# Optimization experiments

Hardware: AMD Instinct MI355X
Metric: run time of the kernel (lower is better)

The kernel has to match this reference:

```python
import jax, jax.numpy as jnp
import numpy as np

EPS = 1e-08

def setup_inputs() -> dict:
    key = jax.random.key(0)
    k1, k2 = jax.random.split(key)
    h = jax.random.normal(k1, (4096, 512), dtype=jnp.float32)   # [B, D]
    A = jax.random.normal(k2, (32768, 512), dtype=jnp.float32)  # [K, D]
    return {"h": h, "A": A}

def _l2_normalize(x, eps=EPS):
    # matches torch F.normalize(p=2): x / max(||x||, eps)
    n = jnp.sqrt(jnp.sum(x * x, axis=-1, keepdims=True))
    return x / jnp.maximum(n, eps)

def reference(h, A):
    # cosine metric: normalize both, matmul, argmax over K
    h_n = _l2_normalize(h)                      # [B, D]
    A_n = _l2_normalize(A)                      # [K, D]
    scores = jnp.einsum('bd,kd->bk', h_n, A_n)  # [B, K]
    idx = jnp.argmax(scores, axis=1, keepdims=True)  # [B, 1] int
    return idx
```

## Files before the change

kernel.cpp:

```cpp
#include <hip/hip_runtime.h>
#include <stdint.h>


#define DIM 512
#define B_ROWS 4096
#define K_ROWS 32768
#define BT 128
#define KT 128
#define NKT (K_ROWS / KT)
#define KSLOTS 32
#define NCHUNK 4
#define QSCALE (127.0f / 0.26f)

typedef __attribute__((ext_vector_type(4))) float fx4;
typedef __attribute__((ext_vector_type(4))) int int4v;
typedef unsigned long long u64;

__device__ __forceinline__ uint32_t ford(float s) {
    uint32_t u = __float_as_uint(s);
    return u ^ ((uint32_t)((int32_t)u >> 31) | 0x80000000u);
}
__device__ __forceinline__ u64 umax64(u64 a, u64 b) { return a > b ? a : b; }
__device__ __forceinline__ u64 umin64(u64 a, u64 b) { return a < b ? a : b; }
__device__ __forceinline__ uint32_t umax32(uint32_t a, uint32_t b) { return a > b ? a : b; }
__device__ __forceinline__ uint32_t umin32(uint32_t a, uint32_t b) { return a < b ? a : b; }

__device__ __forceinline__ int q8(float x, float qs) {
    int v = __float2int_rn(x * qs);
    return v < -127 ? -127 : (v > 127 ? 127 : v);
}

__global__ __launch_bounds__(256) void prep_kernel(const float* __restrict__ A,
                                                   const float* __restrict__ h,
                                                   char* __restrict__ a8,
                                                   char* __restrict__ h8,
                                                   float* __restrict__ rn) {
    const int lane = threadIdx.x & 63, wid = threadIdx.x >> 6;
    const bool isA = blockIdx.x < 8192;
    const int row = (isA ? blockIdx.x : blockIdx.x - 8192) * 4 + wid;
    const float* src = (isA ? A : h) + (size_t)row * DIM;
    char* dst = (isA ? a8 : h8) + (size_t)row * DIM;

    const fx4* p = (const fx4*)src;
    fx4 a = p[lane * 2], b = p[lane * 2 + 1];
    float ss = a[0]*a[0] + a[1]*a[1] + a[2]*a[2] + a[3]*a[3]
             + b[0]*b[0] + b[1]*b[1] + b[2]*b[2] + b[3]*b[3];
    #pragma unroll
    for (int off = 32; off > 0; off >>= 1) ss += __shfl_xor(ss, off, 64);
    float r = 1.0f / fmaxf(sqrtf(ss), 1e-8f);
    if (isA && lane == 0) rn[row] = r;

    float qs = r * QSCALE;
    int v0 = q8(a[0], qs), v1 = q8(a[1], qs), v2 = q8(a[2], qs), v3 = q8(a[3], qs);
    int v4 = q8(b[0], qs), v5 = q8(b[1], qs), v6 = q8(b[2], qs), v7 = q8(b[3], qs);
    uint32_t lo = (uint32_t)(v0 & 255) | ((uint32_t)(v1 & 255) << 8)
                | ((uint32_t)(v2 & 255) << 16) | ((uint32_t)(v3 & 255) << 24);
    uint32_t hi = (uint32_t)(v4 & 255) | ((uint32_t)(v5 & 255) << 8)
                | ((uint32_t)(v6 & 255) << 16) | ((uint32_t)(v7 & 255) << 24);
    *reinterpret_cast<uint2*>(dst + lane * 8) = make_uint2(lo, hi);
}

typedef __attribute__((address_space(3))) uint32_t lds_u32;
typedef __attribute__((address_space(1))) const uint32_t g_u32;

__global__ __launch_bounds__(256, 2) void score_kernel(
    const char* __restrict__ h8, const char* __restrict__ a8,
    u64* __restrict__ cand)
{
    __shared__ __attribute__((aligned(16))) char smem[65536];

    const int t = threadIdx.x, lane = t & 63, wid = t >> 6;
    const int wm = wid >> 1, wn = wid & 1;
    const int lr = lane & 15, q = lane >> 4;
    const int btile = blockIdx.x >> 5, kslot = blockIdx.x & 31;
    const int b0 = btile * BT;

    const int srow = lane >> 3;
    const int scol = (lane & 7) ^ srow;
    const int s7 = lr & 7;
    const int sw0 = (q ^ s7) * 16;
    const int sw1 = ((4 + q) ^ s7) * 16;

    const char* hsrc = h8 + (size_t)b0 * DIM;

    uint32_t v1[16], v2[16];
    #pragma unroll
    for (int s = 0; s < 16; s++) { v1[s] = 0u; v2[s] = 0u; }

    auto stage = [&](int cc, int buf) {
        const int kt = kslot + (cc >> 2) * KSLOTS;
        const int dcc = cc & 3;
        const char* asrc = a8 + (size_t)(kt * KT) * DIM;
        char* hb = smem + buf * 32768;
        char* ab = hb + 16384;
        #pragma unroll
        for (int i = 0; i < 4; i++) {
            int issue = wid * 4 + i;
            size_t roff = (size_t)(issue * 8 + srow) * DIM + dcc * 128 + scol * 16;
            __builtin_amdgcn_global_load_lds((g_u32*)(hsrc + roff),
                (lds_u32*)(hb + issue * 1024), 16, 0, 0);
            __builtin_amdgcn_global_load_lds((g_u32*)(asrc + roff),
                (lds_u32*)(ab + issue * 1024), 16, 0, 0);
        }
    };

    stage(0, 0);

    #pragma unroll 1
    for (int it = 0; it < 8; it++) {
        int4v acc[4][4];
        #pragma unroll
        for (int mi = 0; mi < 4; mi++)
            #pragma unroll
            for (int ni = 0; ni < 4; ni++)
                acc[mi][ni] = (int4v){0, 0, 0, 0};

        #pragma unroll
        for (int dc = 0; dc < 4; dc++) {
            const int c = it * 4 + dc;
            if (dc < 3 || it < 7) stage(c + 1, (dc & 1) ^ 1);

            if (dc < 3 || it < 7) {
                asm volatile("s_waitcnt vmcnt(8)" ::: "memory");
            } else {
                asm volatile("s_waitcnt vmcnt(0)" ::: "memory");
            }
            __builtin_amdgcn_s_barrier();

            const char* hf = smem + (dc & 1) * 32768;
            const char* af = hf + 16384;

            int4v af0[4], af1[4];
            #pragma unroll
            for (int ni = 0; ni < 4; ni++) {
                const char* base = af + (wn * 64 + ni * 16 + lr) * 128;
                af0[ni] = *reinterpret_cast<const int4v*>(base + sw0);
                af1[ni] = *reinterpret_cast<const int4v*>(base + sw1);
            }
            __builtin_amdgcn_s_setprio(1);
            #pragma unroll
            for (int mi = 0; mi < 4; mi++) {
                const char* base = hf + (wm * 64 + mi * 16 + lr) * 128;
                int4v h0 = *reinterpret_cast<const int4v*>(base + sw0);
                int4v h1 = *reinterpret_cast<const int4v*>(base + sw1);
                #pragma unroll
                for (int ni = 0; ni < 4; ni++) {
                    acc[mi][ni] = __builtin_amdgcn_mfma_i32_16x16x64_i8(h0, af0[ni], acc[mi][ni], 0, 0, 0);
                    acc[mi][ni] = __builtin_amdgcn_mfma_i32_16x16x64_i8(h1, af1[ni], acc[mi][ni], 0, 0, 0);
                }
            }
            __builtin_amdgcn_s_setprio(0);

            if (dc == 3) {
                const uint32_t metabase = (uint32_t)(it << 2);
                #pragma unroll
                for (int mi = 0; mi < 4; mi++)
                    #pragma unroll
                    for (int ni = 0; ni < 4; ni++) {
                        const uint32_t meta = metabase | (uint32_t)ni;
                        #pragma unroll
                        for (int r = 0; r < 4; r++) {
                            uint32_t ord = (uint32_t)acc[mi][ni][r] ^ 0x80000000u;
                            uint32_t pk = (ord & 0xFFFFFFC0u) | meta;
                            int s = mi * 4 + r;
                            uint32_t lo = umin32(v1[s], pk);
                            v1[s] = umax32(v1[s], pk);
                            v2[s] = umax32(v2[s], lo);
                        }
                    }
            }

            asm volatile("s_waitcnt lgkmcnt(0)" ::: "memory");
            __builtin_amdgcn_s_barrier();
        }
    }

    uint32_t* cl = (uint32_t*)smem;
    u64 g1 = 0, g2 = 0, g3 = 0;
    for (int pass = 0; pass < 2; pass++) {
        __syncthreads();
        #pragma unroll
        for (int s = 0; s < 16; s++) {
            int mi = s >> 2, r = s & 3;
            int row_local = wm * 64 + mi * 16 + q * 4 + r;
            cl[row_local * 33 + wn * 16 + lr] = pass ? v2[s] : v1[s];
        }
        __syncthreads();
        if (t < BT) {
            #pragma unroll 4
            for (int j = 0; j < 32; j++) {
                uint32_t pv = cl[t * 33 + j];
                uint32_t meta = pv & 63u;
                int k = (kslot + (int)(meta >> 2) * KSLOTS) * KT
                      + (j >> 4) * 64 + (int)(meta & 3u) * 16 + (j & 15);
                u64 e = ((u64)(pv & 0xFFFFFFC0u) << 32) | (u64)(~(uint32_t)k);
                u64 t1 = umax64(g1, e), t2 = umin64(g1, e);
                g3 = umax64(g3, umin64(g2, t2));
                g2 = umax64(g2, t2);
                g1 = t1;
            }
        }
    }
    if (t < BT) {
        size_t base = ((size_t)(b0 + t) * KSLOTS + kslot) * 3;
        cand[base] = g1;
        cand[base + 1] = g2;
        cand[base + 2] = g3;
    }
}

__global__ __launch_bounds__(256) void refine_kernel(
    const float* __restrict__ h, const float* __restrict__ A,
    const float* __restrict__ rn, const u64* __restrict__ cand,
    int* __restrict__ out)
{
    const int t = threadIdx.x, lane = t & 63, wid = t >> 6;
    const int row = blockIdx.x * 4 + wid;
    const u64* cr = cand + (size_t)row * (KSLOTS * 3);
    u64 x0 = cr[lane];
    u64 x1 = (lane < KSLOTS * 3 - 64) ? cr[64 + lane] : 0ULL;

    u64 sel[8];
    #pragma unroll
    for (int j = 0; j < 8; j++) {
        u64 v = umax64(x0, x1);
        #pragma unroll
        for (int m = 32; m >= 1; m >>= 1) v = umax64(v, __shfl_xor(v, m, 64));
        sel[j] = v;
        if (x0 == v) x0 = 0;
        else if (x1 == v) x1 = 0;
    }

    const fx4* hp = reinterpret_cast<const fx4*>(h + (size_t)row * DIM);
    fx4 h0 = hp[lane * 2], h1 = hp[lane * 2 + 1];

    u64 best = 0;
    #pragma unroll
    for (int j = 0; j < 8; j++) {
        uint32_t kg = ~(uint32_t)sel[j];
        const fx4* ap = reinterpret_cast<const fx4*>(A + (size_t)kg * DIM);
        fx4 a0 = ap[lane * 2], a1 = ap[lane * 2 + 1];
        float s = h0[0]*a0[0] + h0[1]*a0[1] + h0[2]*a0[2] + h0[3]*a0[3]
                + h1[0]*a1[0] + h1[1]*a1[1] + h1[2]*a1[2] + h1[3]*a1[3];
        #pragma unroll
        for (int m = 32; m >= 1; m >>= 1) s += __shfl_xor(s, m, 64);
        s *= rn[kg];
        u64 pk = ((u64)ford(s) << 32) | (u64)(~kg);
        best = umax64(best, pk);
    }
    if (lane == 0) out[row] = (int)(~(uint32_t)best);
}

extern "C" void kernel_launch(void* const* d_in, const int* in_sizes, int n_in,
                              void* d_out, int out_size, void* d_ws, size_t ws_size,
                              hipStream_t stream) {
    const float* h = (const float*)d_in[0];
    const float* A = (const float*)d_in[1];
    int* out = (int*)d_out;

    char* w = (char*)d_ws;
    char* a8 = w;
    char* h8 = w + (size_t)K_ROWS * DIM;
    float* rn = (float*)(w + (size_t)(K_ROWS + B_ROWS) * DIM);
    u64* cand = (u64*)(w + (size_t)(K_ROWS + B_ROWS) * DIM
                         + (size_t)K_ROWS * sizeof(float));

    prep_kernel<<<8192 + 1024, 256, 0, stream>>>(A, h, a8, h8, rn);
    score_kernel<<<32 * KSLOTS, 256, 0, stream>>>(h8, a8, cand);
    refine_kernel<<<B_ROWS / 4, 256, 0, stream>>>(h, A, rn, cand, out);
}
```

Baseline: 195.4 us.

## Fuse prep, score and refine into one cooperative kernel with grid syncs

Merges the three launches into one persistent cooperative kernel of 512 blocks. Between phases it uses grid-wide barriers, and each block runs two score units in sequence. The aim is to remove launch gaps and kernel-boundary drains. In exchange, the score phase loses the scheduler's dynamic load balancing and becomes a fixed two-wave schedule. Prep and refine now run in strided loops over fewer waves, and grid.sync adds its own cost. If the cooperative launch fails, the code falls back to the original three kernels.

Result: slower. 337.7 us (+72.8%).

```diff
diff --git a/kernel.cpp b/kernel.cpp
--- a/kernel.cpp
+++ b/kernel.cpp
@@ -1,5 +1,8 @@
 #include <hip/hip_runtime.h>
+#include <hip/hip_cooperative_groups.h>
 #include <stdint.h>
+
+namespace cg = cooperative_groups;
 
 
 #define DIM 512
@@ -9,7 +12,6 @@
 #define KT 128
 #define NKT (K_ROWS / KT)
 #define KSLOTS 32
-#define NCHUNK 4
 #define QSCALE (127.0f / 0.26f)
 
 typedef __attribute__((ext_vector_type(4))) float fx4;
@@ -30,14 +32,18 @@
     return v < -127 ? -127 : (v > 127 ? 127 : v);
 }
 
-__global__ __launch_bounds__(256) void prep_kernel(const float* __restrict__ A,
-                                                   const float* __restrict__ h,
-                                                   char* __restrict__ a8,
-                                                   char* __restrict__ h8,
-                                                   float* __restrict__ rn) {
-    const int lane = threadIdx.x & 63, wid = threadIdx.x >> 6;
-    const bool isA = blockIdx.x < 8192;
-    const int row = (isA ? blockIdx.x : blockIdx.x - 8192) * 4 + wid;
+typedef __attribute__((address_space(3))) uint32_t lds_u32;
+typedef __attribute__((address_space(1))) const uint32_t g_u32;
+
+
+__device__ __forceinline__ void prep_row(const float* __restrict__ A,
+                                         const float* __restrict__ h,
+                                         char* __restrict__ a8,
+                                         char* __restrict__ h8,
+                                         float* __restrict__ rn,
+                                         int r , int lane) {
+    const bool isA = r < K_ROWS;
+    const int row = isA ? r : r - K_ROWS;
     const float* src = (isA ? A : h) + (size_t)row * DIM;
     char* dst = (isA ? a8 : h8) + (size_t)row * DIM;
 
@@ -47,10 +53,10 @@
              + b[0]*b[0] + b[1]*b[1] + b[2]*b[2] + b[3]*b[3];
     #pragma unroll
     for (int off = 32; off > 0; off >>= 1) ss += __shfl_xor(ss, off, 64);
-    float r = 1.0f / fmaxf(sqrtf(ss), 1e-8f);
-    if (isA && lane == 0) rn[row] = r;
-
-    float qs = r * QSCALE;
+    float r1 = 1.0f / fmaxf(sqrtf(ss), 1e-8f);
+    if (isA && lane == 0) rn[row] = r1;
+
+    float qs = r1 * QSCALE;
     int v0 = q8(a[0], qs), v1 = q8(a[1], qs), v2 = q8(a[2], qs), v3 = q8(a[3], qs);
     int v4 = q8(b[0], qs), v5 = q8(b[1], qs), v6 = q8(b[2], qs), v7 = q8(b[3], qs);
     uint32_t lo = (uint32_t)(v0 & 255) | ((uint32_t)(v1 & 255) << 8)
@@ -60,19 +66,14 @@
     *reinterpret_cast<uint2*>(dst + lane * 8) = make_uint2(lo, hi);
 }
 
-typedef __attribute__((address_space(3))) uint32_t lds_u32;
-typedef __attribute__((address_space(1))) const uint32_t g_u32;
-
-__global__ __launch_bounds__(256, 2) void score_kernel(
-    const char* __restrict__ h8, const char* __restrict__ a8,
-    u64* __restrict__ cand)
-{
-    __shared__ __attribute__((aligned(16))) char smem[65536];
-
-    const int t = threadIdx.x, lane = t & 63, wid = t >> 6;
+__device__ __forceinline__ void score_unit(const char* __restrict__ h8,
+                                           const char* __restrict__ a8,
+                                           u64* __restrict__ cand,
+                                           char* smem, int unit,
+                                           int t, int lane, int wid) {
     const int wm = wid >> 1, wn = wid & 1;
     const int lr = lane & 15, q = lane >> 4;
-    const int btile = blockIdx.x >> 5, kslot = blockIdx.x & 31;
+    const int btile = unit >> 5, kslot = unit & 31;
     const int b0 = btile * BT;
 
     const int srow = lane >> 3;
@@ -176,14 +177,15 @@
     }
 
     uint32_t* cl = (uint32_t*)smem;
+    const int wm_ = wid >> 1, wn_ = wid & 1;
     u64 g1 = 0, g2 = 0, g3 = 0;
     for (int pass = 0; pass < 2; pass++) {
         __syncthreads();
         #pragma unroll
         for (int s = 0; s < 16; s++) {
             int mi = s >> 2, r = s & 3;
-            int row_local = wm * 64 + mi * 16 + q * 4 + r;
-            cl[row_local * 33 + wn * 16 + lr] = pass ? v2[s] : v1[s];
+            int row_local = wm_ * 64 + mi * 16 + q * 4 + r;
+            cl[row_local * 33 + wn_ * 16 + lr] = pass ? v2[s] : v1[s];
         }
         __syncthreads();
         if (t < BT) {
@@ -209,13 +211,12 @@
     }
 }
 
-__global__ __launch_bounds__(256) void refine_kernel(
-    const float* __restrict__ h, const float* __restrict__ A,
-    const float* __restrict__ rn, const u64* __restrict__ cand,
-    int* __restrict__ out)
-{
-    const int t = threadIdx.x, lane = t & 63, wid = t >> 6;
-    const int row = blockIdx.x * 4 + wid;
+__device__ __forceinline__ void refine_row(const float* __restrict__ h,
+                                           const float* __restrict__ A,
+                                           const float* __restrict__ rn,
+                                           const u64* __restrict__ cand,
+                                           int* __restrict__ out,
+                                           int row, int lane) {
     const u64* cr = cand + (size_t)row * (KSLOTS * 3);
     u64 x0 = cr[lane];
     u64 x1 = (lane < KSLOTS * 3 - 64) ? cr[64 + lane] : 0ULL;
@@ -251,6 +252,69 @@
     if (lane == 0) out[row] = (int)(~(uint32_t)best);
 }
 
+
+__global__ __launch_bounds__(256, 2) void fused_kernel(
+    const float* __restrict__ h, const float* __restrict__ A,
+    char* __restrict__ a8, char* __restrict__ h8, float* __restrict__ rn,
+    u64* __restrict__ cand, int* __restrict__ out)
+{
+    __shared__ __attribute__((aligned(16))) char smem[65536];
+    const int t = threadIdx.x, lane = t & 63, wid = t >> 6;
+    cg::grid_group grid = cg::this_grid();
+
+    {
+        const int wgid = blockIdx.x * 4 + wid;
+        #pragma unroll 1
+        for (int r = wgid; r < K_ROWS + B_ROWS; r += 2048)
+            prep_row(A, h, a8, h8, rn, r, lane);
+    }
+    grid.sync();
+
+    #pragma unroll 1
+    for (int u = 0; u < 2; u++) {
+        __syncthreads();
+        score_unit(h8, a8, cand, smem, blockIdx.x * 2 + u, t, lane, wid);
+    }
+    grid.sync();
+
+    {
+        const int wgid = blockIdx.x * 4 + wid;
+        #pragma unroll 1
+        for (int row = wgid; row < B_ROWS; row += 2048)
+            refine_row(h, A, rn, cand, out, row, lane);
+    }
+}
+
+
+__global__ __launch_bounds__(256) void prep_kernel(const float* __restrict__ A,
+                                                   const float* __restrict__ h,
+                                                   char* __restrict__ a8,
+                                                   char* __restrict__ h8,
+                                                   float* __restrict__ rn) {
+    const int lane = threadIdx.x & 63, wid = threadIdx.x >> 6;
+    const bool isA = blockIdx.x < 8192;
+    const int r = (isA ? blockIdx.x : blockIdx.x - 8192) * 4 + wid + (isA ? 0 : K_ROWS);
+    prep_row(A, h, a8, h8, rn, r, lane);
+}
+
+__global__ __launch_bounds__(256, 2) void score_kernel(
+    const char* __restrict__ h8, const char* __restrict__ a8,
+    u64* __restrict__ cand)
+{
+    __shared__ __attribute__((aligned(16))) char smem[65536];
+    const int t = threadIdx.x, lane = t & 63, wid = t >> 6;
+    score_unit(h8, a8, cand, smem, blockIdx.x, t, lane, wid);
+}
+
+__global__ __launch_bounds__(256) void refine_kernel(
+    const float* __restrict__ h, const float* __restrict__ A,
+    const float* __restrict__ rn, const u64* __restrict__ cand,
+    int* __restrict__ out)
+{
+    const int t = threadIdx.x, lane = t & 63, wid = t >> 6;
+    refine_row(h, A, rn, cand, out, blockIdx.x * 4 + wid, lane);
+}
+
 extern "C" void kernel_launch(void* const* d_in, const int* in_sizes, int n_in,
                               void* d_out, int out_size, void* d_ws, size_t ws_size,
                               hipStream_t stream) {
@@ -265,7 +329,15 @@
     u64* cand = (u64*)(w + (size_t)(K_ROWS + B_ROWS) * DIM
                          + (size_t)K_ROWS * sizeof(float));
 
-    prep_kernel<<<8192 + 1024, 256, 0, stream>>>(A, h, a8, h8, rn);
-    score_kernel<<<32 * KSLOTS, 256, 0, stream>>>(h8, a8, cand);
-    refine_kernel<<<B_ROWS / 4, 256, 0, stream>>>(h, A, rn, cand, out);
-}
+    void* args[] = { (void*)&h, (void*)&A, (void*)&a8, (void*)&h8,
+                     (void*)&rn, (void*)&cand, (void*)&out };
+    hipError_t err = hipLaunchCooperativeKernel(
+        reinterpret_cast<const void*>(&fused_kernel),
+        dim3(512), dim3(256), args, 0, stream);
+
+    if (err != hipSuccess) {
+        prep_kernel<<<8192 + 1024, 256, 0, stream>>>(A, h, a8, h8, rn);
+        score_kernel<<<32 * KSLOTS, 256, 0, stream>>>(h8, a8, cand);
+        refine_kernel<<<B_ROWS / 4, 256, 0, stream>>>(h, A, rn, cand, out);
+    }
+}
```
